# Optimization experiments

Hardware: AMD Instinct MI355X
Metric: run time of the kernel (lower is better)

## Reference

```python
import jax, jax.numpy as jnp
import numpy as np

C = 256
NUM_HEADS = 4


def setup_inputs() -> dict:
    key = jax.random.key(0)
    ks = jax.random.split(key, 7)
    B, H, W = 4, 64, 64
    s = 1.0 / np.sqrt(C)
    return {
        "x": jax.random.normal(ks[0], (B, C, H, W), dtype=jnp.float32),
        "ln_gamma": jnp.ones((C,), jnp.float32),
        "ln_beta": jnp.zeros((C,), jnp.float32),
        "w_qkv": jax.random.normal(ks[1], (C, 3 * C), dtype=jnp.float32) * s,
        "b_qkv": jnp.zeros((3 * C,), jnp.float32),
        "w_proj": jax.random.normal(ks[2], (C, C), dtype=jnp.float32) * s,
        "b_proj": jnp.zeros((C,), jnp.float32),
    }


def reference(x, ln_gamma, ln_beta, w_qkv, b_qkv, w_proj, b_proj):
    B, Cc, H, W = x.shape
    N = H * W
    hd = Cc // NUM_HEADS
    # [B, N, C] token layout
    x_ = jnp.transpose(x, (0, 2, 3, 1)).reshape(B, N, Cc)
    # LayerNorm over channel dim
    mu = jnp.mean(x_, axis=-1, keepdims=True)
    var = jnp.mean(jnp.square(x_ - mu), axis=-1, keepdims=True)
    xn = (x_ - mu) * jax.lax.rsqrt(var + 1e-5) * ln_gamma + ln_beta
    qkv = xn @ w_qkv + b_qkv  # [B, N, 3C]
    q, k, v = jnp.split(qkv, 3, axis=-1)
    # [B, heads, N, hd]
    q = q.reshape(B, N, NUM_HEADS, hd).transpose(0, 2, 1, 3)
    k = k.reshape(B, N, NUM_HEADS, hd).transpose(0, 2, 1, 3)
    v = v.reshape(B, N, NUM_HEADS, hd).transpose(0, 2, 1, 3)
    # NOTE: source scales by 1/sqrt(C), not 1/sqrt(head_dim)
    scores = jnp.einsum("bhnd,bhmd->bhnm", q, k) / jnp.sqrt(jnp.float32(Cc))
    attn = jax.nn.softmax(scores, axis=-1)
    out = jnp.einsum("bhnm,bhmd->bhnd", attn, v)
    out = out.transpose(0, 2, 1, 3).reshape(B, N, Cc)
    out = out @ w_proj + b_proj
    out = out.reshape(B, H, W, Cc).transpose(0, 3, 1, 2)
    return x + out
```

## Files before the change

### kernel.cpp

```cpp
#include <hip/hip_runtime.h>
#include <hip/hip_bf16.h>

typedef __bf16 bf16_t;
typedef bf16_t bf16x8 __attribute__((ext_vector_type(8)));
typedef bf16_t bf16x4v __attribute__((ext_vector_type(4)));
typedef float f32x4 __attribute__((ext_vector_type(4)));
typedef float f32x16 __attribute__((ext_vector_type(16)));
typedef int i32x4 __attribute__((ext_vector_type(4)));
typedef int i32x2 __attribute__((ext_vector_type(2)));

constexpr int C = 256;
constexpr int Bb = 4;
constexpr int N = 4096;
constexpr int NH = 4;
constexpr int HD = 64;
constexpr float SM_SCALE_LOG2E = 0.0625f * 1.44269504088896340736f;

__device__ __forceinline__ int swz_chunk(int row, int chunk) {
  return row * 128 + ((chunk ^ (row & 7)) << 4);
}

__device__ __forceinline__ f32x4 mfma16(bf16x8 a, bf16x8 b, f32x4 c) {
  return __builtin_amdgcn_mfma_f32_16x16x32_bf16(a, b, c, 0, 0, 0);
}
__device__ __forceinline__ f32x16 mfma32(bf16x8 a, bf16x8 b, f32x16 c) {
  return __builtin_amdgcn_mfma_f32_32x32x16_bf16(a, b, c, 0, 0, 0);
}

__device__ __forceinline__ int cvt_pk_bf16(float lo, float hi) {
  int d;
  asm("v_cvt_pk_bf16_f32 %0, %1, %2" : "=v"(d) : "v"(lo), "v"(hi));
  return d;
}
__device__ __forceinline__ i32x2 plswap(int a, int b) {
  return __builtin_amdgcn_permlane32_swap(a, b, false, false);
}
__device__ __forceinline__ float xhalf_max(float v) {
  i32x2 r = plswap(__float_as_int(v), __float_as_int(v));
  return fmaxf(__int_as_float(r[0]), __int_as_float(r[1]));
}
__device__ __forceinline__ float xhalf_sum(float v) {
  i32x2 r = plswap(__float_as_int(v), __float_as_int(v));
  return __int_as_float(r[0]) + __int_as_float(r[1]);
}

__global__ __launch_bounds__(256, 2) void ln_kernel(
    const float* __restrict__ x, const float* __restrict__ gamma,
    const float* __restrict__ beta, bf16_t* __restrict__ xn) {
  __shared__ float tile[256][65];
  __shared__ float red[2][4][64];
  __shared__ float mu_s[64], rs_s[64];
  int tid = threadIdx.x, lane = tid & 63, wv = tid >> 6;
  int b = blockIdx.x >> 6;
  int n0 = (blockIdx.x & 63) << 6;
  const float* xb = x + ((size_t)b * C) * N + n0;
  #pragma unroll 4
  for (int i = 0; i < 64; ++i) {
    int c = wv * 64 + i;
    tile[c][lane] = xb[(size_t)c * N + lane];
  }
  __syncthreads();
  float s = 0.f, s2 = 0.f;
  #pragma unroll 8
  for (int i = 0; i < 64; ++i) {
    float v = tile[wv * 64 + i][lane];
    s += v; s2 += v * v;
  }
  red[0][wv][lane] = s; red[1][wv][lane] = s2;
  __syncthreads();
  if (tid < 64) {
    float ts  = red[0][0][tid] + red[0][1][tid] + red[0][2][tid] + red[0][3][tid];
    float ts2 = red[1][0][tid] + red[1][1][tid] + red[1][2][tid] + red[1][3][tid];
    float mu  = ts * (1.f / 256.f);
    float var = fmaxf(ts2 * (1.f / 256.f) - mu * mu, 0.f);
    mu_s[tid] = mu;
    rs_s[tid] = rsqrtf(var + 1e-5f);
  }
  __syncthreads();
  float g = gamma[tid], be = beta[tid];
  bf16_t* xo = xn + ((size_t)(b * N + n0)) * C + tid;
  #pragma unroll 4
  for (int i = 0; i < 64; ++i) {
    float v = (tile[tid][i] - mu_s[i]) * rs_s[i] * g + be;
    xo[(size_t)i * C] = (bf16_t)v;
  }
}

__global__ void conv_w(const float* __restrict__ wqkv, const float* __restrict__ wproj,
                       bf16_t* __restrict__ wqkvT, bf16_t* __restrict__ wprojT) {
  int id = blockIdx.x * 256 + threadIdx.x;
  if (id < 768 * 256) {
    int nn = id >> 8, kk = id & 255;
    wqkvT[id] = (bf16_t)wqkv[(size_t)kk * 768 + nn];
  }
  if (id < 256 * 256) {
    int nn = id >> 8, kk = id & 255;
    wprojT[id] = (bf16_t)wproj[(size_t)kk * 256 + nn];
  }
}

__global__ __launch_bounds__(256, 4) void gemm_qkv(
    const bf16_t* __restrict__ xn, const bf16_t* __restrict__ wT,
    const float* __restrict__ bias,
    bf16_t* __restrict__ Q, bf16_t* __restrict__ K, bf16_t* __restrict__ Vt) {
  __shared__ char smem[2 * 8192];
  char* As = smem;
  char* Bs = smem + 8192;
  int tid = threadIdx.x, lane = tid & 63, wv = tid >> 6;
  int mt = blockIdx.x & 255, nt = blockIdx.x >> 8;
  int m0 = mt * 64, ncol0 = nt * 64;
  f32x4 acc[4];
  #pragma unroll
  for (int i = 0; i < 4; ++i) acc[i] = (f32x4){0.f, 0.f, 0.f, 0.f};
  for (int kt = 0; kt < 4; ++kt) {
    int k0 = kt * 64;
    __syncthreads();
    #pragma unroll
    for (int it = 0; it < 2; ++it) {
      int idx = it * 256 + tid, row = idx >> 3, cb = idx & 7;
      *(i32x4*)(As + swz_chunk(row, cb)) =
          *(const i32x4*)(xn + (size_t)(m0 + row) * C + k0 + cb * 8);
      *(i32x4*)(Bs + swz_chunk(row, cb)) =
          *(const i32x4*)(wT + (size_t)(ncol0 + row) * C + k0 + cb * 8);
    }
    __syncthreads();
    int r = wv * 16 + (lane & 15), q = lane >> 4;
    bf16x8 a0 = *(const bf16x8*)(As + swz_chunk(r, q));
    bf16x8 a1 = *(const bf16x8*)(As + swz_chunk(r, 4 + q));
    #pragma unroll
    for (int ct = 0; ct < 4; ++ct) {
      int br = ct * 16 + (lane & 15);
      bf16x8 b0 = *(const bf16x8*)(Bs + swz_chunk(br, q));
      bf16x8 b1 = *(const bf16x8*)(Bs + swz_chunk(br, 4 + q));
      acc[ct] = mfma16(a0, b0, acc[ct]);
      acc[ct] = mfma16(a1, b1, acc[ct]);
    }
  }
  #pragma unroll
  for (int ct = 0; ct < 4; ++ct) {
    int cg = ncol0 + ct * 16 + (lane & 15);
    float bv = bias[cg];
    int sect = cg >> 8;
    int cc = cg & 255;
    int h = cc >> 6, d = cc & 63;
    #pragma unroll
    for (int j = 0; j < 4; ++j) {
      int m = m0 + wv * 16 + (lane >> 4) * 4 + j;
      int b_ = m >> 12, n = m & 4095;
      float v = acc[ct][j] + bv;
      if (sect == 0) {
        Q[((size_t)((b_ * NH + h) * N + n)) * HD + d] = (bf16_t)(v * SM_SCALE_LOG2E);
      } else if (sect == 1) {
        K[((size_t)((b_ * NH + h) * N + n)) * HD + d] = (bf16_t)v;
      } else {
        Vt[((size_t)((b_ * NH + h) * HD + d)) * N + n] = (bf16_t)v;
      }
    }
  }
}

__global__ __launch_bounds__(512, 4) void attn_kernel(
    const bf16_t* __restrict__ Q, const bf16_t* __restrict__ K,
    const bf16_t* __restrict__ Vt, bf16_t* __restrict__ aout) {
  __shared__ char smem[34816];
  char* tiles = smem;
  int tid = threadIdx.x, lane = tid & 63, wv = tid >> 6;
  int hi = lane >> 5, qL = lane & 31;
  int wq = wv >> 1, par = wv & 1;
  int bh = blockIdx.x >> 5, qt = blockIdx.x & 31;
  int q0 = qt * 128;

  const bf16_t* Kbh = K + (size_t)bh * N * HD;
  const bf16_t* Vbh = Vt + (size_t)bh * HD * N;
  int srow = tid >> 3, scb = tid & 7;
  int sd = swz_chunk(srow, scb);

  i32x4 st0 = *(const i32x4*)(Kbh + (size_t)srow * HD + scb * 8);
  i32x4 st1 = *(const i32x4*)(Vbh + (size_t)srow * N + scb * 8);
  i32x4 st2 = *(const i32x4*)(Kbh + (size_t)(64 + srow) * HD + scb * 8);
  i32x4 st3 = *(const i32x4*)(Vbh + (size_t)srow * N + 64 + scb * 8);

  const bf16_t* Qbase = Q + ((size_t)bh * N + q0) * HD;
  #pragma unroll
  for (int it = 0; it < 2; ++it) {
    int idx = it * 512 + tid;
    int row = idx >> 3, cb = idx & 7;
    *(i32x4*)(tiles + swz_chunk(row, cb)) =
        *(const i32x4*)(Qbase + (size_t)row * HD + cb * 8);
  }
  __syncthreads();
  bf16x8 qb[4];
  #pragma unroll
  for (int hs = 0; hs < 4; ++hs)
    qb[hs] = *(const bf16x8*)(tiles + swz_chunk(wq * 32 + qL, hs * 2 + hi));
  __syncthreads();

  char* kbase = tiles + par * 16384;
  char* vbase = kbase + 8192;

  float m_r = -3.0e38f, l_r = 0.f;
  f32x16 o0, o1;
  #pragma unroll
  for (int i = 0; i < 16; ++i) { o0[i] = 0.f; o1[i] = 0.f; }

  for (int adv = 0; adv < 32; ++adv) {
    *(i32x4*)(tiles + sd)         = st0;
    *(i32x4*)(tiles + 8192 + sd)  = st1;
    *(i32x4*)(tiles + 16384 + sd) = st2;
    *(i32x4*)(tiles + 24576 + sd) = st3;
    __syncthreads();
    if (adv < 31) {
      int n1 = (adv + 1) * 128;
      st0 = *(const i32x4*)(Kbh + (size_t)(n1 + srow) * HD + scb * 8);
      st1 = *(const i32x4*)(Vbh + (size_t)srow * N + n1 + scb * 8);
      st2 = *(const i32x4*)(Kbh + (size_t)(n1 + 64 + srow) * HD + scb * 8);
      st3 = *(const i32x4*)(Vbh + (size_t)srow * N + n1 + 64 + scb * 8);
    }
    f32x16 s0, s1;
    #pragma unroll
    for (int i = 0; i < 16; ++i) { s0[i] = 0.f; s1[i] = 0.f; }
    #pragma unroll
    for (int hs = 0; hs < 4; ++hs) {
      bf16x8 ka0 = *(const bf16x8*)(kbase + swz_chunk(qL, hs * 2 + hi));
      bf16x8 ka1 = *(const bf16x8*)(kbase + swz_chunk(32 + qL, hs * 2 + hi));
      s0 = mfma32(ka0, qb[hs], s0);
      s1 = mfma32(ka1, qb[hs], s1);
    }
    float tm = s0[0];
    #pragma unroll
    for (int i = 1; i < 16; ++i) tm = fmaxf(tm, s0[i]);
    #pragma unroll
    for (int i = 0; i < 16; ++i) tm = fmaxf(tm, s1[i]);
    tm = xhalf_max(tm);
    float nm = fmaxf(m_r, tm);
    if (!__all(nm == m_r)) {
      float f = __builtin_amdgcn_exp2f(m_r - nm);
      l_r *= f;
      o0 *= f; o1 *= f;
      m_r = nm;
    }
    float rs = 0.f;
    #pragma unroll
    for (int i = 0; i < 16; ++i) {
      float p = __builtin_amdgcn_exp2f(s0[i] - m_r); s0[i] = p; rs += p;
    }
    #pragma unroll
    for (int i = 0; i < 16; ++i) {
      float p = __builtin_amdgcn_exp2f(s1[i] - m_r); s1[i] = p; rs += p;
    }
    l_r += xhalf_sum(rs);
    #pragma unroll
    for (int t16 = 0; t16 < 4; ++t16) {
      int dE0, dE1, dO0, dO1;
      if (t16 < 2) {
        dE0 = cvt_pk_bf16(s0[t16 * 8 + 0], s0[t16 * 8 + 1]);
        dE1 = cvt_pk_bf16(s0[t16 * 8 + 2], s0[t16 * 8 + 3]);
        dO0 = cvt_pk_bf16(s0[t16 * 8 + 4], s0[t16 * 8 + 5]);
        dO1 = cvt_pk_bf16(s0[t16 * 8 + 6], s0[t16 * 8 + 7]);
      } else {
        dE0 = cvt_pk_bf16(s1[(t16 - 2) * 8 + 0], s1[(t16 - 2) * 8 + 1]);
        dE1 = cvt_pk_bf16(s1[(t16 - 2) * 8 + 2], s1[(t16 - 2) * 8 + 3]);
        dO0 = cvt_pk_bf16(s1[(t16 - 2) * 8 + 4], s1[(t16 - 2) * 8 + 5]);
        dO1 = cvt_pk_bf16(s1[(t16 - 2) * 8 + 6], s1[(t16 - 2) * 8 + 7]);
      }
      i32x2 rA = plswap(dE0, dO0);
      i32x2 rB = plswap(dE1, dO1);
      union { i32x4 i; bf16x8 h; } u;
      u.i = (i32x4){rA[0], rB[0], rA[1], rB[1]};
      bf16x8 va0 = *(const bf16x8*)(vbase + swz_chunk(qL, t16 * 2 + hi));
      bf16x8 va1 = *(const bf16x8*)(vbase + swz_chunk(32 + qL, t16 * 2 + hi));
      o0 = mfma32(va0, u.h, o0);
      o1 = mfma32(va1, u.h, o1);
    }
    __syncthreads();
  }

  float* mlb = (float*)(smem + 32768);
  if (hi == 0) {
    mlb[(wv * 32 + qL) * 2]     = m_r;
    mlb[(wv * 32 + qL) * 2 + 1] = l_r;
  }
  __syncthreads();
  float m_p = mlb[((wv ^ 1) * 32 + qL) * 2];
  float l_p = mlb[((wv ^ 1) * 32 + qL) * 2 + 1];
  float M = fmaxf(m_r, m_p);
  float w_s = __builtin_amdgcn_exp2f(m_r - M);
  float l_tot = l_r * w_s + l_p * __builtin_amdgcn_exp2f(m_p - M);
  char* obuf = smem + wq * 8192;
  if (par == 0) {
    #pragma unroll
    for (int g = 0; g < 8; ++g) {
      f32x4 t;
      #pragma unroll
      for (int j = 0; j < 4; ++j)
        t[j] = (g < 4 ? o0[g * 4 + j] : o1[(g - 4) * 4 + j]) * w_s;
      *(f32x4*)(obuf + swz_chunk(lane, g)) = t;
    }
  }
  __syncthreads();
  if (par == 1) {
    float inv = 1.f / l_tot;
    int qglob = q0 + wq * 32 + qL;
    int b_ = bh >> 2, h = bh & 3;
    bf16_t* ab = aout + ((size_t)b_ * N + qglob) * C + h * HD;
    #pragma unroll
    for (int g = 0; g < 8; ++g) {
      f32x4 part = *(const f32x4*)(obuf + swz_chunk(lane, g));
      int hdb = g >> 2, gg = g & 3;
      bf16x4v ov;
      #pragma unroll
      for (int j = 0; j < 4; ++j) {
        float own = hdb ? o1[gg * 4 + j] : o0[gg * 4 + j];
        ov[j] = (bf16_t)((part[j] + own * w_s) * inv);
      }
      *(bf16x4v*)(ab + hdb * 32 + gg * 8 + hi * 4) = ov;
    }
  }
}

__global__ __launch_bounds__(256, 4) void gemm_proj(
    const bf16_t* __restrict__ aout, const bf16_t* __restrict__ wT,
    const float* __restrict__ bias, const float* __restrict__ x,
    float* __restrict__ out) {
  __shared__ char smem[2 * 8192];
  char* As = smem;
  char* Bs = smem + 8192;
  int tid = threadIdx.x, lane = tid & 63, wv = tid >> 6;
  int mt = blockIdx.x & 255, nt = blockIdx.x >> 8;
  int m0 = mt * 64, c0 = nt * 64;
  f32x4 acc[4];
  #pragma unroll
  for (int i = 0; i < 4; ++i) acc[i] = (f32x4){0.f, 0.f, 0.f, 0.f};
  for (int kt = 0; kt < 4; ++kt) {
    int k0 = kt * 64;
    __syncthreads();
    #pragma unroll
    for (int it = 0; it < 2; ++it) {
      int idx = it * 256 + tid, row = idx >> 3, cb = idx & 7;
      *(i32x4*)(As + swz_chunk(row, cb)) =
          *(const i32x4*)(aout + (size_t)(m0 + row) * C + k0 + cb * 8);
      *(i32x4*)(Bs + swz_chunk(row, cb)) =
          *(const i32x4*)(wT + (size_t)(c0 + row) * C + k0 + cb * 8);
    }
    __syncthreads();
    int r = wv * 16 + (lane & 15), q = lane >> 4;
    bf16x8 a0 = *(const bf16x8*)(As + swz_chunk(r, q));
    bf16x8 a1 = *(const bf16x8*)(As + swz_chunk(r, 4 + q));
    #pragma unroll
    for (int ct = 0; ct < 4; ++ct) {
      int br = ct * 16 + (lane & 15);
      bf16x8 b0 = *(const bf16x8*)(Bs + swz_chunk(br, q));
      bf16x8 b1 = *(const bf16x8*)(Bs + swz_chunk(br, 4 + q));
      acc[ct] = mfma16(a0, b0, acc[ct]);
      acc[ct] = mfma16(a1, b1, acc[ct]);
    }
  }
  #pragma unroll
  for (int ct = 0; ct < 4; ++ct) {
    int c = c0 + ct * 16 + (lane & 15);
    float bv = bias[c];
    int m = m0 + wv * 16 + (lane >> 4) * 4;
    int b_ = m >> 12, n = m & 4095;
    size_t off = ((size_t)(b_ * C + c)) * N + n;
    f32x4 xin = *(const f32x4*)(x + off);
    f32x4 res;
    #pragma unroll
    for (int j = 0; j < 4; ++j) res[j] = xin[j] + acc[ct][j] + bv;
    *(f32x4*)(out + off) = res;
  }
}

extern "C" void kernel_launch(void* const* d_in, const int* in_sizes, int n_in,
                              void* d_out, int out_size, void* d_ws, size_t ws_size,
                              hipStream_t stream) {
  const float* x     = (const float*)d_in[0];
  const float* gam   = (const float*)d_in[1];
  const float* bet   = (const float*)d_in[2];
  const float* wqkv  = (const float*)d_in[3];
  const float* bqkv  = (const float*)d_in[4];
  const float* wproj = (const float*)d_in[5];
  const float* bproj = (const float*)d_in[6];
  float* out = (float*)d_out;

  char* ws = (char*)d_ws;
  size_t off = 0;
  auto alloc = [&](size_t bytes) {
    void* p = ws + off;
    off += (bytes + 255) & ~(size_t)255;
    return p;
  };
  bf16_t* xn     = (bf16_t*)alloc((size_t)Bb * N * C * 2);
  bf16_t* wqkvT  = (bf16_t*)alloc((size_t)768 * 256 * 2);
  bf16_t* wprojT = (bf16_t*)alloc((size_t)256 * 256 * 2);
  bf16_t* Qb     = (bf16_t*)alloc((size_t)Bb * NH * N * HD * 2);
  bf16_t* Kb     = (bf16_t*)alloc((size_t)Bb * NH * N * HD * 2);
  bf16_t* Vtb    = (bf16_t*)alloc((size_t)Bb * NH * HD * N * 2);
  bf16_t* aout   = (bf16_t*)alloc((size_t)Bb * N * C * 2);
  if (ws_size < off) return;

  hipLaunchKernelGGL(ln_kernel, dim3(Bb * 64), dim3(256), 0, stream, x, gam, bet, xn);
  hipLaunchKernelGGL(conv_w, dim3(768), dim3(256), 0, stream, wqkv, wproj, wqkvT, wprojT);
  hipLaunchKernelGGL(gemm_qkv, dim3(256 * 12), dim3(256), 0, stream, xn, wqkvT, bqkv,
                     Qb, Kb, Vtb);
  hipLaunchKernelGGL(attn_kernel, dim3(16 * 32), dim3(512), 0, stream,
                     Qb, Kb, Vtb, aout);
  hipLaunchKernelGGL(gemm_proj, dim3(256 * 4), dim3(256), 0, stream, aout, wprojT,
                     bproj, x, out);
}
```

Baseline: 208.6 us.

## Double-buffer attention K/V via direct global-to-LDS loads and enlarge QKV GEMM tiles

The attention kernel now loads K/V tiles straight into LDS with global_load_lds into a double buffer, which removes the register staging and one barrier per iteration. It also uses a tree max reduction and a lazy rescale that only updates the running max when it grows by more than 8 (log2 units). The QKV GEMM moves from 64x64 to 128x128 tiles with a 4x4 MFMA tile per wave for more operand reuse. The costs are doubled LDS in attention (lower occupancy) and the lazy-rescale threshold, which allows exp2 values up to 256 before renormalisation.

```diff
diff --git a/kernel.cpp b/kernel.cpp
--- a/kernel.cpp
+++ b/kernel.cpp
@@ -25,6 +25,12 @@
 }
 __device__ __forceinline__ f32x16 mfma32(bf16x8 a, bf16x8 b, f32x16 c) {
   return __builtin_amdgcn_mfma_f32_32x32x16_bf16(a, b, c, 0, 0, 0);
+}
+
+__device__ __forceinline__ void glds16(const void* g, void* l) {
+  __builtin_amdgcn_global_load_lds(
+      (const __attribute__((address_space(1))) void*)g,
+      (__attribute__((address_space(3))) void*)l, 16, 0, 0);
 }
 
 __device__ __forceinline__ int cvt_pk_bf16(float lo, float hi) {
@@ -99,24 +105,28 @@
   }
 }
 
-__global__ __launch_bounds__(256, 4) void gemm_qkv(
+__global__ __launch_bounds__(256, 2) void gemm_qkv(
     const bf16_t* __restrict__ xn, const bf16_t* __restrict__ wT,
     const float* __restrict__ bias,
     bf16_t* __restrict__ Q, bf16_t* __restrict__ K, bf16_t* __restrict__ Vt) {
-  __shared__ char smem[2 * 8192];
+  __shared__ char smem[32768];
   char* As = smem;
-  char* Bs = smem + 8192;
+  char* Bs = smem + 16384;
   int tid = threadIdx.x, lane = tid & 63, wv = tid >> 6;
-  int mt = blockIdx.x & 255, nt = blockIdx.x >> 8;
-  int m0 = mt * 64, ncol0 = nt * 64;
-  f32x4 acc[4];
-  #pragma unroll
-  for (int i = 0; i < 4; ++i) acc[i] = (f32x4){0.f, 0.f, 0.f, 0.f};
+  int mt = blockIdx.x & 127, nt = blockIdx.x >> 7;
+  int m0 = mt * 128, ncol0 = nt * 128;
+  int wr = wv >> 1, wc = wv & 1;
+  f32x4 acc[4][4];
+  #pragma unroll
+  for (int i = 0; i < 4; ++i)
+    #pragma unroll
+    for (int j = 0; j < 4; ++j) acc[i][j] = (f32x4){0.f, 0.f, 0.f, 0.f};
+  int q = lane >> 4;
   for (int kt = 0; kt < 4; ++kt) {
     int k0 = kt * 64;
     __syncthreads();
     #pragma unroll
-    for (int it = 0; it < 2; ++it) {
+    for (int it = 0; it < 4; ++it) {
       int idx = it * 256 + tid, row = idx >> 3, cb = idx & 7;
       *(i32x4*)(As + swz_chunk(row, cb)) =
           *(const i32x4*)(xn + (size_t)(m0 + row) * C + k0 + cb * 8);
@@ -124,36 +134,45 @@
           *(const i32x4*)(wT + (size_t)(ncol0 + row) * C + k0 + cb * 8);
     }
     __syncthreads();
-    int r = wv * 16 + (lane & 15), q = lane >> 4;
-    bf16x8 a0 = *(const bf16x8*)(As + swz_chunk(r, q));
-    bf16x8 a1 = *(const bf16x8*)(As + swz_chunk(r, 4 + q));
-    #pragma unroll
-    for (int ct = 0; ct < 4; ++ct) {
-      int br = ct * 16 + (lane & 15);
+    bf16x8 a[4][2];
+    #pragma unroll
+    for (int mi = 0; mi < 4; ++mi) {
+      int ar = wr * 64 + mi * 16 + (lane & 15);
+      a[mi][0] = *(const bf16x8*)(As + swz_chunk(ar, q));
+      a[mi][1] = *(const bf16x8*)(As + swz_chunk(ar, 4 + q));
+    }
+    #pragma unroll
+    for (int ci = 0; ci < 4; ++ci) {
+      int br = wc * 64 + ci * 16 + (lane & 15);
       bf16x8 b0 = *(const bf16x8*)(Bs + swz_chunk(br, q));
       bf16x8 b1 = *(const bf16x8*)(Bs + swz_chunk(br, 4 + q));
-      acc[ct] = mfma16(a0, b0, acc[ct]);
-      acc[ct] = mfma16(a1, b1, acc[ct]);
-    }
-  }
-  #pragma unroll
-  for (int ct = 0; ct < 4; ++ct) {
-    int cg = ncol0 + ct * 16 + (lane & 15);
+      #pragma unroll
+      for (int mi = 0; mi < 4; ++mi) {
+        acc[mi][ci] = mfma16(a[mi][1], b1, mfma16(a[mi][0], b0, acc[mi][ci]));
+      }
+    }
+  }
+  #pragma unroll
+  for (int ci = 0; ci < 4; ++ci) {
+    int cg = ncol0 + wc * 64 + ci * 16 + (lane & 15);
     float bv = bias[cg];
     int sect = cg >> 8;
     int cc = cg & 255;
     int h = cc >> 6, d = cc & 63;
     #pragma unroll
-    for (int j = 0; j < 4; ++j) {
-      int m = m0 + wv * 16 + (lane >> 4) * 4 + j;
-      int b_ = m >> 12, n = m & 4095;
-      float v = acc[ct][j] + bv;
-      if (sect == 0) {
-        Q[((size_t)((b_ * NH + h) * N + n)) * HD + d] = (bf16_t)(v * SM_SCALE_LOG2E);
-      } else if (sect == 1) {
-        K[((size_t)((b_ * NH + h) * N + n)) * HD + d] = (bf16_t)v;
-      } else {
-        Vt[((size_t)((b_ * NH + h) * HD + d)) * N + n] = (bf16_t)v;
+    for (int mi = 0; mi < 4; ++mi) {
+      #pragma unroll
+      for (int j = 0; j < 4; ++j) {
+        int m = m0 + wr * 64 + mi * 16 + (lane >> 4) * 4 + j;
+        int b_ = m >> 12, n = m & 4095;
+        float v = acc[mi][ci][j] + bv;
+        if (sect == 0) {
+          Q[((size_t)((b_ * NH + h) * N + n)) * HD + d] = (bf16_t)(v * SM_SCALE_LOG2E);
+        } else if (sect == 1) {
+          K[((size_t)((b_ * NH + h) * N + n)) * HD + d] = (bf16_t)v;
+        } else {
+          Vt[((size_t)((b_ * NH + h) * HD + d)) * N + n] = (bf16_t)v;
+        }
       }
     }
   }
@@ -162,8 +181,7 @@
 __global__ __launch_bounds__(512, 4) void attn_kernel(
     const bf16_t* __restrict__ Q, const bf16_t* __restrict__ K,
     const bf16_t* __restrict__ Vt, bf16_t* __restrict__ aout) {
-  __shared__ char smem[34816];
-  char* tiles = smem;
+  __shared__ char smem[67584];
   int tid = threadIdx.x, lane = tid & 63, wv = tid >> 6;
   int hi = lane >> 5, qL = lane & 31;
   int wq = wv >> 1, par = wv & 1;
@@ -172,31 +190,30 @@
 
   const bf16_t* Kbh = K + (size_t)bh * N * HD;
   const bf16_t* Vbh = Vt + (size_t)bh * HD * N;
-  int srow = tid >> 3, scb = tid & 7;
-  int sd = swz_chunk(srow, scb);
-
-  i32x4 st0 = *(const i32x4*)(Kbh + (size_t)srow * HD + scb * 8);
-  i32x4 st1 = *(const i32x4*)(Vbh + (size_t)srow * N + scb * 8);
-  i32x4 st2 = *(const i32x4*)(Kbh + (size_t)(64 + srow) * HD + scb * 8);
-  i32x4 st3 = *(const i32x4*)(Vbh + (size_t)srow * N + 64 + scb * 8);
-
+  int sr = tid >> 3;
+  int sc = (tid & 7) ^ (sr & 7);
+
+  {
+    char* lb = smem;
+    glds16(Kbh + (size_t)sr * HD + sc * 8,            lb + tid * 16);
+    glds16(Vbh + (size_t)sr * N + sc * 8,             lb + 8192 + tid * 16);
+    glds16(Kbh + (size_t)(64 + sr) * HD + sc * 8,     lb + 16384 + tid * 16);
+    glds16(Vbh + (size_t)sr * N + 64 + sc * 8,        lb + 24576 + tid * 16);
+  }
+  char* Qt = smem + 32768;
   const bf16_t* Qbase = Q + ((size_t)bh * N + q0) * HD;
   #pragma unroll
   for (int it = 0; it < 2; ++it) {
     int idx = it * 512 + tid;
     int row = idx >> 3, cb = idx & 7;
-    *(i32x4*)(tiles + swz_chunk(row, cb)) =
+    *(i32x4*)(Qt + swz_chunk(row, cb)) =
         *(const i32x4*)(Qbase + (size_t)row * HD + cb * 8);
   }
   __syncthreads();
   bf16x8 qb[4];
   #pragma unroll
   for (int hs = 0; hs < 4; ++hs)
-    qb[hs] = *(const bf16x8*)(tiles + swz_chunk(wq * 32 + qL, hs * 2 + hi));
-  __syncthreads();
-
-  char* kbase = tiles + par * 16384;
-  char* vbase = kbase + 8192;
+    qb[hs] = *(const bf16x8*)(Qt + swz_chunk(wq * 32 + qL, hs * 2 + hi));
 
   float m_r = -3.0e38f, l_r = 0.f;
   f32x16 o0, o1;
@@ -204,18 +221,17 @@
   for (int i = 0; i < 16; ++i) { o0[i] = 0.f; o1[i] = 0.f; }
 
   for (int adv = 0; adv < 32; ++adv) {
-    *(i32x4*)(tiles + sd)         = st0;
-    *(i32x4*)(tiles + 8192 + sd)  = st1;
-    *(i32x4*)(tiles + 16384 + sd) = st2;
-    *(i32x4*)(tiles + 24576 + sd) = st3;
     __syncthreads();
     if (adv < 31) {
       int n1 = (adv + 1) * 128;
-      st0 = *(const i32x4*)(Kbh + (size_t)(n1 + srow) * HD + scb * 8);
-      st1 = *(const i32x4*)(Vbh + (size_t)srow * N + n1 + scb * 8);
-      st2 = *(const i32x4*)(Kbh + (size_t)(n1 + 64 + srow) * HD + scb * 8);
-      st3 = *(const i32x4*)(Vbh + (size_t)srow * N + n1 + 64 + scb * 8);
-    }
+      char* lb = smem + (((adv + 1) & 1) << 15);
+      glds16(Kbh + (size_t)(n1 + sr) * HD + sc * 8,        lb + tid * 16);
+      glds16(Vbh + (size_t)sr * N + n1 + sc * 8,           lb + 8192 + tid * 16);
+      glds16(Kbh + (size_t)(n1 + 64 + sr) * HD + sc * 8,   lb + 16384 + tid * 16);
+      glds16(Vbh + (size_t)sr * N + n1 + 64 + sc * 8,      lb + 24576 + tid * 16);
+    }
+    char* kbase = smem + ((adv & 1) << 15) + par * 16384;
+    char* vbase = kbase + 8192;
     f32x16 s0, s1;
     #pragma unroll
     for (int i = 0; i < 16; ++i) { s0[i] = 0.f; s1[i] = 0.f; }
@@ -226,14 +242,19 @@
       s0 = mfma32(ka0, qb[hs], s0);
       s1 = mfma32(ka1, qb[hs], s1);
     }
-    float tm = s0[0];
-    #pragma unroll
-    for (int i = 1; i < 16; ++i) tm = fmaxf(tm, s0[i]);
-    #pragma unroll
-    for (int i = 0; i < 16; ++i) tm = fmaxf(tm, s1[i]);
+    float q0m = fmaxf(fmaxf(s0[0], s0[1]), fmaxf(s0[2], s0[3]));
+    float q1m = fmaxf(fmaxf(s0[4], s0[5]), fmaxf(s0[6], s0[7]));
+    float q2m = fmaxf(fmaxf(s0[8], s0[9]), fmaxf(s0[10], s0[11]));
+    float q3m = fmaxf(fmaxf(s0[12], s0[13]), fmaxf(s0[14], s0[15]));
+    float q4m = fmaxf(fmaxf(s1[0], s1[1]), fmaxf(s1[2], s1[3]));
+    float q5m = fmaxf(fmaxf(s1[4], s1[5]), fmaxf(s1[6], s1[7]));
+    float q6m = fmaxf(fmaxf(s1[8], s1[9]), fmaxf(s1[10], s1[11]));
+    float q7m = fmaxf(fmaxf(s1[12], s1[13]), fmaxf(s1[14], s1[15]));
+    float tm = fmaxf(fmaxf(fmaxf(q0m, q1m), fmaxf(q2m, q3m)),
+                     fmaxf(fmaxf(q4m, q5m), fmaxf(q6m, q7m)));
     tm = xhalf_max(tm);
-    float nm = fmaxf(m_r, tm);
-    if (!__all(nm == m_r)) {
+    if (!__all(tm - m_r <= 8.f)) {
+      float nm = fmaxf(m_r, tm);
       float f = __builtin_amdgcn_exp2f(m_r - nm);
       l_r *= f;
       o0 *= f; o1 *= f;
@@ -272,10 +293,10 @@
       o0 = mfma32(va0, u.h, o0);
       o1 = mfma32(va1, u.h, o1);
     }
-    __syncthreads();
-  }
-
-  float* mlb = (float*)(smem + 32768);
+  }
+
+  __syncthreads();
+  float* mlb = (float*)(smem + 65536);
   if (hi == 0) {
     mlb[(wv * 32 + qL) * 2]     = m_r;
     mlb[(wv * 32 + qL) * 2 + 1] = l_r;
@@ -400,7 +421,7 @@
 
   hipLaunchKernelGGL(ln_kernel, dim3(Bb * 64), dim3(256), 0, stream, x, gam, bet, xn);
   hipLaunchKernelGGL(conv_w, dim3(768), dim3(256), 0, stream, wqkv, wproj, wqkvT, wprojT);
-  hipLaunchKernelGGL(gemm_qkv, dim3(256 * 12), dim3(256), 0, stream, xn, wqkvT, bqkv,
+  hipLaunchKernelGGL(gemm_qkv, dim3(128 * 6), dim3(256), 0, stream, xn, wqkvT, bqkv,
                      Qb, Kb, Vtb);
   hipLaunchKernelGGL(attn_kernel, dim3(16 * 32), dim3(512), 0, stream,
                      Qb, Kb, Vtb, aout);
```

After: 198.7 us. 1.05x faster.
